# Kernel tuning notes

Measured on AMD Instinct MI355X. Metric: run time of the kernel, lower is better.

The kernel has to match this reference:

```python
import jax, jax.numpy as jnp
import numpy as np

PASSES = 6
S = 2           # numEdgeSets
D = 256         # inputLayerSize
OUT = 10        # outputLayerSize
HID = 80
B, N, E = 4, 10000, 160000


def _leaky(x):
    return jax.nn.leaky_relu(x, negative_slope=0.01)


def setup_inputs() -> dict:
    key = jax.random.key(0)
    ks = jax.random.split(key, 18)
    sc = 0.05
    return {
        "nodes": jax.random.normal(ks[0], (B, N, D), jnp.float32),
        "edges": jax.random.randint(ks[1], (B, S, E, 2), 0, N, jnp.int32),
        "problem_type": jax.random.uniform(ks[2], (B, 1), jnp.float32),
        # GRUCell params (torch layout: [3D, D] for ih and hh)
        "gru_w_ih": jax.random.normal(ks[3], (3 * D, D), jnp.float32) * sc,
        "gru_w_hh": jax.random.normal(ks[4], (3 * D, D), jnp.float32) * sc,
        "gru_b_ih": jax.random.normal(ks[5], (3 * D,), jnp.float32) * sc,
        "gru_b_hh": jax.random.normal(ks[6], (3 * D,), jnp.float32) * sc,
        # per-edge-set 2-layer MLP, stacked over edge sets
        "edge_w1": jax.random.normal(ks[7], (S, D, D), jnp.float32) * sc,
        "edge_b1": jax.random.normal(ks[8], (S, D), jnp.float32) * sc,
        "edge_w2": jax.random.normal(ks[9], (S, D, D), jnp.float32) * sc,
        "edge_b2": jax.random.normal(ks[10], (S, D), jnp.float32) * sc,
        # readout head
        "fc1_w": jax.random.normal(ks[11], (HID, D + 1), jnp.float32) * sc,
        "fc1_b": jax.random.normal(ks[12], (HID,), jnp.float32) * sc,
        "fc2_w": jax.random.normal(ks[13], (HID, HID), jnp.float32) * sc,
        "fc2_b": jax.random.normal(ks[14], (HID,), jnp.float32) * sc,
        "fc3_w": jax.random.normal(ks[15], (OUT, HID), jnp.float32) * sc,
        "fc3_b": jax.random.normal(ks[16], (OUT,), jnp.float32) * sc,
    }


def _gru_cell(x, h, w_ih, w_hh, b_ih, b_hh):
    # torch.nn.GRUCell semantics; x,h: [B,N,D]
    gi = jnp.einsum("bnd,ed->bne", x, w_ih) + b_ih   # [B,N,3D]
    gh = jnp.einsum("bnd,ed->bne", h, w_hh) + b_hh
    i_r, i_z, i_n = jnp.split(gi, 3, axis=-1)
    h_r, h_z, h_n = jnp.split(gh, 3, axis=-1)
    r = jax.nn.sigmoid(i_r + h_r)
    z = jax.nn.sigmoid(i_z + h_z)
    n = jnp.tanh(i_n + r * h_n)
    return (1.0 - z) * n + z * h


def reference(nodes, edges, problem_type, gru_w_ih, gru_w_hh, gru_b_ih, gru_b_hh,
              edge_w1, edge_b1, edge_w2, edge_b2,
              fc1_w, fc1_b, fc2_w, fc2_b, fc3_w, fc3_b):
    bidx = jnp.arange(B)[:, None]  # [B,1] for batched scatter
    h = nodes
    for j in range(PASSES):
        incoming = jnp.zeros_like(h)
        for si in range(S):
            dst = edges[:, si, :, 0]  # [B,E]
            src = edges[:, si, :, 1]  # [B,E]
            gathered = jnp.take_along_axis(h, src[:, :, None], axis=1)  # [B,E,D]
            y = _leaky(jnp.einsum("bed,fd->bef", gathered, edge_w1[si]) + edge_b1[si])
            y = jnp.einsum("bed,fd->bef", y, edge_w2[si]) + edge_b2[si]
            incoming = incoming.at[bidx, dst].add(y)
        h = _gru_cell(incoming, h, gru_w_ih, gru_w_hh, gru_b_ih, gru_b_hh)
        if j < PASSES - 2:
            h = jax.lax.stop_gradient(h)  # mirrors .detach()
    # graph readout: sum over nodes, log, nan->0, relu, +inf->finite max
    s = jnp.sum(h, axis=1)               # [B,D]
    l = jnp.log(s)
    l = jnp.where(jnp.isnan(l), 0.0, l)
    l = jax.nn.relu(l)
    finite_max = jnp.max(jnp.where(jnp.isinf(l), -jnp.inf, l), axis=1, keepdims=True)
    l = jnp.where(jnp.isinf(l), finite_max, l)
    x = jnp.concatenate([l, problem_type], axis=1)  # [B,D+1]
    x = _leaky(x @ fc1_w.T + fc1_b)
    x = _leaky(x @ fc2_w.T + fc2_b)
    return x @ fc3_w.T + fc3_b  # [B,OUT]
```

## Files before the change

kernel.cpp:

```cpp
#include <hip/hip_runtime.h>
#include <math.h>

#define NNODES 10000
#define NEDGES 160000
#define DIM    256
#define BATCH  4
#define NG     8
#define MROWS  40064
#define RBLK   625
#define RGRP   79
#define RBLK128 313
#define RGRP128 40

typedef __attribute__((ext_vector_type(8))) __bf16 bf16x8;
typedef __attribute__((ext_vector_type(4))) float  floatx4;
typedef __attribute__((ext_vector_type(8))) unsigned short ushort8v;

__device__ __forceinline__ float leakyf(float x){ return x > 0.f ? x : 0.01f*x; }
__device__ __forceinline__ float fsig(float x){ return 1.f/(1.f + __expf(-x)); }
__device__ __forceinline__ float ftanh(float x){ return 1.f - 2.f/(1.f + __expf(2.f*x)); }
__device__ __forceinline__ unsigned short f2bf_u(float x){
  unsigned int u = __float_as_uint(x);
  u += 0x7fffu + ((u >> 16) & 1u);
  return (unsigned short)(u >> 16);
}
__device__ __forceinline__ float bfdec(unsigned short u){
  return __uint_as_float(((unsigned int)u) << 16);
}
#define GATE_SCL 65535.f
#define GATE_INV 1.5259021896696422e-5f

#define VMCNT4 asm volatile("s_waitcnt vmcnt(4)" ::: "memory")
#define VMCNT3 asm volatile("s_waitcnt vmcnt(3)" ::: "memory")
#define VMCNT0 asm volatile("s_waitcnt vmcnt(0)" ::: "memory")
#define LGKM0  asm volatile("s_waitcnt lgkmcnt(0)" ::: "memory")
#define SBAR   __builtin_amdgcn_s_barrier()
#define SCHEDB __builtin_amdgcn_sched_barrier(0)

__device__ __forceinline__ void glds16(unsigned short* lds, const unsigned short* g){
  __builtin_amdgcn_global_load_lds(
      (const __attribute__((address_space(1))) void*)g,
      (__attribute__((address_space(3))) void*)lds, 16, 0, 0);
}

__global__ void ihinit_kernel(const float* __restrict__ nodes,
                              unsigned short* __restrict__ ihcat,
                              unsigned short* __restrict__ h_lo){
  int idx = blockIdx.x*256 + threadIdx.x;
  int row = idx >> 8, d = idx & 255;
  float v = nodes[idx];
  unsigned short h = f2bf_u(v);
  ihcat[(size_t)row*512 + 256 + d] = h;
  h_lo[idx] = f2bf_u(v - bfdec(h));
}

__global__ void w1cat_kernel(const float* __restrict__ ew1, unsigned short* __restrict__ o){
  int idx = blockIdx.x*256 + threadIdx.x;
  int n = idx >> 8, k = idx & 255;
  o[idx] = f2bf_u(ew1[(n>>8)*65536 + (n&255)*256 + k]);
}
__global__ void w2k_kernel(const float* __restrict__ ew2, unsigned short* __restrict__ o){
  int idx = blockIdx.x*256 + threadIdx.x;
  int n = idx >> 10, kp = idx & 1023;
  int j = kp & 511, term = kp >> 9;
  int si = j >> 8, k = j & 255;
  float v = ew2[si*65536 + n*256 + k];
  unsigned short h = f2bf_u(v);
  o[idx] = term ? f2bf_u(v - bfdec(h)) : h;
}
__global__ void wk2_kernel(const float* __restrict__ w, unsigned short* __restrict__ o){
  int idx = blockIdx.x*256 + threadIdx.x;
  int c = idx >> 9, kp = idx & 511;
  int k = kp & 255, term = kp >> 8;
  float v = w[c*256 + k];
  unsigned short h = f2bf_u(v);
  o[idx] = term ? f2bf_u(v - bfdec(h)) : h;
}
__global__ void wcomb_kernel(const float* __restrict__ wih, const float* __restrict__ whh,
                             unsigned short* __restrict__ o){
  int idx = blockIdx.x*256 + threadIdx.x;
  int c = idx >> 10, kp = idx & 1023;
  int seg = kp >> 8, k = kp & 255;
  const float* w = (seg & 1) ? whh : wih;
  float v = w[c*256 + k];
  unsigned short h = f2bf_u(v);
  o[idx] = (seg >> 1) ? f2bf_u(v - bfdec(h)) : h;
}

__global__ void hist_kernel(const int* __restrict__ edges, int* __restrict__ cnt){
  int idx = blockIdx.x*256 + threadIdx.x;
  if (idx < NG*NEDGES){
    int g = idx / NEDGES, e = idx - g*NEDGES;
    int d = edges[((size_t)g*NEDGES + e)*2];
    atomicAdd(&cnt[g*NNODES + d], 1);
  }
}

__global__ __launch_bounds__(256) void scan_kernel(const int* __restrict__ cnt, int* __restrict__ off){
  __shared__ int sc[256];
  int g = blockIdx.x, t = threadIdx.x;
  int base = 0;
  for (int c=0;c<40;c++){
    int i = c*256 + t;
    int v = (i < NNODES) ? cnt[g*NNODES + i] : 0;
    __syncthreads();
    sc[t] = v;
    __syncthreads();
    for (int o=1;o<256;o<<=1){
      int u = (t>=o) ? sc[t-o] : 0;
      __syncthreads();
      sc[t] += u;
      __syncthreads();
    }
    if (i < NNODES) off[g*(NNODES+1) + i] = base + sc[t] - v;
    base += sc[255];
  }
  if (t == 0) off[g*(NNODES+1) + NNODES] = base;
}

__global__ void scatter_kernel(const int* __restrict__ edges, const int* __restrict__ off,
                               int* __restrict__ cur, int* __restrict__ ssrc){
  int idx = blockIdx.x*256 + threadIdx.x;
  if (idx < NG*NEDGES){
    int g = idx / NEDGES, e = idx - g*NEDGES;
    const int* ep = &edges[((size_t)g*NEDGES + e)*2];
    int d = ep[0], s = ep[1];
    int pos = off[g*(NNODES+1) + d] + atomicAdd(&cur[g*NNODES + d], 1);
    ssrc[g*NEDGES + pos] = s;
  }
}

template<int KP, int RS, int KM>
__device__ __forceinline__ void mm128_core(
    const unsigned short* __restrict__ Ab, const unsigned short* __restrict__ Wb,
    unsigned short* lds, floatx4 (&acc)[4][2])
{
  const int t = threadIdx.x;
  const int w = t >> 6, lane = t & 63;
  const int q = lane >> 4, col = lane & 15;
  const int wr = (w >> 2) * 64;
  const int wc = (w & 3) * 32;
  const int sr = t >> 3;
  const int sk = ((t & 7) ^ (sr & 7)) * 8;

  auto STAGE = [&](int kb, int buf){
    unsigned short* Al = lds + buf*16384;
    unsigned short* Bl = Al + 8192;
    #pragma unroll
    for (int i=0;i<2;i++){
      int r = i*64 + sr;
      glds16(&Al[i*4096 + w*512], &Ab[(size_t)r*RS + ((kb + sk) & KM)]);
      glds16(&Bl[i*4096 + w*512], &Wb[(size_t)r*KP + kb + sk]);
    }
  };

  STAGE(0, 0);
  int cur = 0;
  #pragma unroll
  for (int kb = 0; kb < KP; kb += 64){
    if (kb + 64 < KP){
      STAGE(kb + 64, cur^1);
      VMCNT4;
    } else {
      VMCNT0;
    }
    SBAR; SCHEDB;
    const unsigned short* Al = lds + cur*16384;
    const unsigned short* Bl = Al + 8192;
    #pragma unroll
    for (int ks2=0; ks2<2; ks2++){
      bf16x8 a[4], bf[2];
      #pragma unroll
      for (int mi=0;mi<4;mi++){
        int r = wr + mi*16 + col;
        int j = (ks2*4 + q) ^ (r & 7);
        a[mi] = *(const bf16x8*)&Al[r*64 + j*8];
      }
      #pragma unroll
      for (int ni=0;ni<2;ni++){
        int r = wc + ni*16 + col;
        int j = (ks2*4 + q) ^ (r & 7);
        bf[ni] = *(const bf16x8*)&Bl[r*64 + j*8];
      }
      #pragma unroll
      for (int mi=0;mi<4;mi++)
        #pragma unroll
        for (int ni=0;ni<2;ni++)
          acc[mi][ni] = __builtin_amdgcn_mfma_f32_16x16x32_bf16(a[mi], bf[ni], acc[mi][ni], 0,0,0);
    }
    SCHEDB; LGKM0; SBAR;
    cur ^= 1;
  }
}

__device__ __forceinline__ void mm64x2_core(
    const unsigned short* __restrict__ A1, const unsigned short* __restrict__ W1,
    const unsigned short* __restrict__ A2, const unsigned short* __restrict__ W2,
    unsigned short* lds, floatx4 (&ai)[4], floatx4 (&ah)[4])
{
  const int t = threadIdx.x;
  const int w = t >> 6, lane = t & 63;
  const int q = lane >> 4, col = lane & 15;
  const int wc = w*16;
  const int sr = t >> 3;
  const int sk = ((t & 7) ^ (sr & 7)) * 8;

  auto STAGE = [&](int s, int buf){
    const unsigned short* A = (s < 8) ? A1 : A2;
    const unsigned short* W = (s < 8) ? W1 : W2;
    int kb = (s & 7) * 64;
    unsigned short* Al = lds + buf*12288;
    unsigned short* Bl = Al + 4096;
    glds16(&Al[w*512], &A[(size_t)sr*512 + ((kb + sk) & 255)]);
    #pragma unroll
    for (int i=0;i<2;i++){
      int r = i*64 + sr;
      glds16(&Bl[i*4096 + w*512], &W[(size_t)r*512 + kb + sk]);
    }
  };

  STAGE(0, 0);
  int cur = 0;
  #pragma unroll
  for (int s = 0; s < 16; s++){
    if (s < 15){
      STAGE(s + 1, cur^1);
      VMCNT3;
    } else {
      VMCNT0;
    }
    SBAR; SCHEDB;
    const unsigned short* Al = lds + cur*12288;
    const unsigned short* Bl = Al + 4096;
    #pragma unroll
    for (int ks2=0; ks2<2; ks2++){
      bf16x8 a[4], bf;
      #pragma unroll
      for (int mi=0;mi<4;mi++){
        int r = mi*16 + col;
        int j = (ks2*4 + q) ^ (r & 7);
        a[mi] = *(const bf16x8*)&Al[r*64 + j*8];
      }
      {
        int r = wc + col;
        int j = (ks2*4 + q) ^ (r & 7);
        bf = *(const bf16x8*)&Bl[r*64 + j*8];
      }
      if (s < 8){
        #pragma unroll
        for (int mi=0;mi<4;mi++)
          ai[mi] = __builtin_amdgcn_mfma_f32_16x16x32_bf16(a[mi], bf, ai[mi], 0,0,0);
      } else {
        #pragma unroll
        for (int mi=0;mi<4;mi++)
          ah[mi] = __builtin_amdgcn_mfma_f32_16x16x32_bf16(a[mi], bf, ah[mi], 0,0,0);
      }
    }
    SCHEDB; LGKM0; SBAR;
    cur ^= 1;
  }
}

#define XDECODE(NCOL) \
  const int bid_ = blockIdx.x; \
  const int rb_ = ((bid_ >> 3) / NCOL) * 8 + (bid_ & 7); \
  const int colb_ = (bid_ >> 3) % NCOL; \
  if (rb_ >= RBLK) return;

#define XDECODE128(NCOL) \
  const int bid_ = blockIdx.x; \
  const int rb_ = ((bid_ >> 3) / NCOL) * 8 + (bid_ & 7); \
  const int colb_ = (bid_ >> 3) % NCOL; \
  if (rb_ >= RBLK128) return;

#define MMPRO128 \
  const int t = threadIdx.x, w = t >> 6, lane = t & 63; \
  const int q = lane >> 4, col = lane & 15; \
  const int wrq = (w >> 2) * 64, wcq = (w & 3) * 32; \
  floatx4 acc[4][2]; \
  _Pragma("unroll") for (int mi=0;mi<4;mi++) _Pragma("unroll") for (int ni=0;ni<2;ni++) \
    acc[mi][ni] = (floatx4){0.f,0.f,0.f,0.f};

__global__ __launch_bounds__(512,4) void z64_kernel(
    const unsigned short* __restrict__ ihcat, const unsigned short* __restrict__ w1cat,
    const float* __restrict__ eb1, unsigned short* __restrict__ Z)
{
  __shared__ unsigned short lds[32768];
  XDECODE128(4)
  const int row0 = rb_*128, col0 = colb_*128;
  MMPRO128
  mm128_core<256,512,255>(ihcat + (size_t)row0*512 + 256, w1cat + (size_t)col0*256, lds, acc);

  #pragma unroll
  for (int ni=0;ni<2;ni++){
    int n = col0 + wcq + ni*16 + col;
    int si = n >> 8, cz = n & 255;
    float bb = eb1[si*256 + cz];
    unsigned short* zp = Z + (size_t)si*MROWS*256 + cz;
    #pragma unroll
    for (int mi=0;mi<4;mi++)
      #pragma unroll
      for (int rr=0;rr<4;rr++){
        int row = row0 + wrq + mi*16 + q*4 + rr;
        zp[(size_t)row*256] = f2bf_u(leakyf(acc[mi][ni][rr] + bb));
      }
  }
}

__global__ __launch_bounds__(256) void aggregate_kernel(
    const unsigned short* __restrict__ Z, const int* __restrict__ ssrc,
    const int* __restrict__ off, unsigned short* __restrict__ Sb)
{
  const int bid = blockIdx.x;
  const int g = bid & 7;
  const int dgrp = bid >> 3;
  const int b = g >> 1, si = g & 1;
  const int w = threadIdx.x >> 6, lane = threadIdx.x & 63;
  const int half = lane >> 5, c = lane & 31;
  const unsigned short* zb = Z + ((size_t)si*MROWS + b*10000)*256 + c*8;
  const int* sp = ssrc + (size_t)g*NEDGES;
  const int* offg = off + g*(NNODES+1);

  #pragma unroll
  for (int p=0;p<2;p++){
    const int d = dgrp*16 + w*4 + p*2 + half;
    int j = offg[d];
    const int j1 = offg[d+1];
    float a0=0.f,a1=0.f,a2=0.f,a3=0.f,a4=0.f,a5=0.f,a6=0.f,a7=0.f;
    for (; j+8 <= j1; j+=8){
      int s[8];
      #pragma unroll
      for (int e=0;e<8;e++) s[e] = sp[j+e];
      ushort8v u[8];
      #pragma unroll
      for (int e=0;e<8;e++) u[e] = *(const ushort8v*)&zb[(size_t)s[e]*256];
      a0 += bfdec(u[0][0])+bfdec(u[1][0])+bfdec(u[2][0])+bfdec(u[3][0]);
      a1 += bfdec(u[0][1])+bfdec(u[1][1])+bfdec(u[2][1])+bfdec(u[3][1]);
      a2 += bfdec(u[0][2])+bfdec(u[1][2])+bfdec(u[2][2])+bfdec(u[3][2]);
      a3 += bfdec(u[0][3])+bfdec(u[1][3])+bfdec(u[2][3])+bfdec(u[3][3]);
      a4 += bfdec(u[0][4])+bfdec(u[1][4])+bfdec(u[2][4])+bfdec(u[3][4]);
      a5 += bfdec(u[0][5])+bfdec(u[1][5])+bfdec(u[2][5])+bfdec(u[3][5]);
      a6 += bfdec(u[0][6])+bfdec(u[1][6])+bfdec(u[2][6])+bfdec(u[3][6]);
      a7 += bfdec(u[0][7])+bfdec(u[1][7])+bfdec(u[2][7])+bfdec(u[3][7]);
      a0 += bfdec(u[4][0])+bfdec(u[5][0])+bfdec(u[6][0])+bfdec(u[7][0]);
      a1 += bfdec(u[4][1])+bfdec(u[5][1])+bfdec(u[6][1])+bfdec(u[7][1]);
      a2 += bfdec(u[4][2])+bfdec(u[5][2])+bfdec(u[6][2])+bfdec(u[7][2]);
      a3 += bfdec(u[4][3])+bfdec(u[5][3])+bfdec(u[6][3])+bfdec(u[7][3]);
      a4 += bfdec(u[4][4])+bfdec(u[5][4])+bfdec(u[6][4])+bfdec(u[7][4]);
      a5 += bfdec(u[4][5])+bfdec(u[5][5])+bfdec(u[6][5])+bfdec(u[7][5]);
      a6 += bfdec(u[4][6])+bfdec(u[5][6])+bfdec(u[6][6])+bfdec(u[7][6]);
      a7 += bfdec(u[4][7])+bfdec(u[5][7])+bfdec(u[6][7])+bfdec(u[7][7]);
    }
    for (; j+4 <= j1; j+=4){
      int s0=sp[j], s1=sp[j+1], s2=sp[j+2], s3=sp[j+3];
      ushort8v u0 = *(const ushort8v*)&zb[(size_t)s0*256];
      ushort8v u1 = *(const ushort8v*)&zb[(size_t)s1*256];
      ushort8v u2 = *(const ushort8v*)&zb[(size_t)s2*256];
      ushort8v u3 = *(const ushort8v*)&zb[(size_t)s3*256];
      a0 += bfdec(u0[0])+bfdec(u1[0])+bfdec(u2[0])+bfdec(u3[0]);
      a1 += bfdec(u0[1])+bfdec(u1[1])+bfdec(u2[1])+bfdec(u3[1]);
      a2 += bfdec(u0[2])+bfdec(u1[2])+bfdec(u2[2])+bfdec(u3[2]);
      a3 += bfdec(u0[3])+bfdec(u1[3])+bfdec(u2[3])+bfdec(u3[3]);
      a4 += bfdec(u0[4])+bfdec(u1[4])+bfdec(u2[4])+bfdec(u3[4]);
      a5 += bfdec(u0[5])+bfdec(u1[5])+bfdec(u2[5])+bfdec(u3[5]);
      a6 += bfdec(u0[6])+bfdec(u1[6])+bfdec(u2[6])+bfdec(u3[6]);
      a7 += bfdec(u0[7])+bfdec(u1[7])+bfdec(u2[7])+bfdec(u3[7]);
    }
    for (; j < j1; j++){
      ushort8v u = *(const ushort8v*)&zb[(size_t)sp[j]*256];
      a0+=bfdec(u[0]); a1+=bfdec(u[1]); a2+=bfdec(u[2]); a3+=bfdec(u[3]);
      a4+=bfdec(u[4]); a5+=bfdec(u[5]); a6+=bfdec(u[6]); a7+=bfdec(u[7]);
    }
    size_t so = (size_t)(b*10000 + d)*512 + si*256 + c*8;
    ushort8v hv;
    hv[0]=f2bf_u(a0); hv[1]=f2bf_u(a1); hv[2]=f2bf_u(a2); hv[3]=f2bf_u(a3);
    hv[4]=f2bf_u(a4); hv[5]=f2bf_u(a5); hv[6]=f2bf_u(a6); hv[7]=f2bf_u(a7);
    *(ushort8v*)&Sb[so] = hv;
  }
}

__global__ __launch_bounds__(512,4) void w264_kernel(
    const unsigned short* __restrict__ Sb, const unsigned short* __restrict__ w2k,
    const float* __restrict__ eb2, const int* __restrict__ off,
    unsigned short* __restrict__ ihcat)
{
  __shared__ unsigned short lds[32768];
  XDECODE128(2)
  const int row0 = rb_*128, col0 = colb_*128;
  MMPRO128
  mm128_core<1024,512,511>(Sb + (size_t)row0*512, w2k + (size_t)col0*1024, lds, acc);

  float b20[2], b21[2];
  #pragma unroll
  for (int ni=0;ni<2;ni++){
    int n = col0 + wcq + ni*16 + col;
    b20[ni] = eb2[n];
    b21[ni] = eb2[256 + n];
  }
  #pragma unroll
  for (int mi=0;mi<4;mi++)
    #pragma unroll
    for (int rr=0;rr<4;rr++){
      int row = row0 + wrq + mi*16 + q*4 + rr;
      int rw = (row < 40000) ? row : 39999;
      int b = rw / 10000, d = rw - b*10000;
      int o0 = (b*2)*(NNODES+1) + d;
      int o1 = (b*2+1)*(NNODES+1) + d;
      float dg0 = (float)(off[o0+1] - off[o0]);
      float dg1 = (float)(off[o1+1] - off[o1]);
      #pragma unroll
      for (int ni=0;ni<2;ni++){
        int n = col0 + wcq + ni*16 + col;
        ihcat[(size_t)row*512 + n] = f2bf_u(acc[mi][ni][rr] + dg0*b20[ni] + dg1*b21[ni]);
      }
    }
}

__global__ __launch_bounds__(512,4) void gruA_kernel(
    const unsigned short* __restrict__ ihcat, const unsigned short* __restrict__ wcomb,
    const float* __restrict__ b_ih, const float* __restrict__ b_hh,
    unsigned short* __restrict__ rz_r, unsigned short* __restrict__ rz_z)
{
  __shared__ unsigned short lds[32768];
  XDECODE128(4)
  const int row0 = rb_*128, col0 = colb_*128;
  MMPRO128
  mm128_core<1024,512,511>(ihcat + (size_t)row0*512, wcomb + (size_t)col0*1024, lds, acc);

  float bb[2];
  #pragma unroll
  for (int ni=0;ni<2;ni++){
    int n = col0 + wcq + ni*16 + col;
    bb[ni] = b_ih[n] + b_hh[n];
  }
  unsigned short* dst = (col0 < 256) ? rz_r : rz_z;
  const int cbase = (col0 & 255) + wcq;
  #pragma unroll
  for (int mi=0;mi<4;mi++)
    #pragma unroll
    for (int rr=0;rr<4;rr++){
      size_t row = (size_t)(row0 + wrq + mi*16 + q*4 + rr);
      #pragma unroll
      for (int ni=0;ni<2;ni++){
        float v = fsig(acc[mi][ni][rr] + bb[ni]);
        dst[row*256 + cbase + ni*16 + col] = (unsigned short)(v*GATE_SCL + 0.5f);
      }
    }
}

__global__ __launch_bounds__(512,4) void gruB_kernel(
    const unsigned short* __restrict__ ihcat, unsigned short* __restrict__ h_lo,
    const unsigned short* __restrict__ wihk, const unsigned short* __restrict__ whhk,
    const float* __restrict__ b_ih, const float* __restrict__ b_hh,
    const unsigned short* __restrict__ rz_r, const unsigned short* __restrict__ rz_z,
    unsigned short* __restrict__ ihcat_nxt)
{
  __shared__ unsigned short lds[24576];
  XDECODE(2)
  const int row0 = rb_*64, dcol0 = colb_*128;
  const int t = threadIdx.x, w = t >> 6, lane = t & 63;
  const int q = lane >> 4, col = lane & 15;

  floatx4 ai[4], ah[4];
  #pragma unroll
  for (int mi=0;mi<4;mi++){ ai[mi] = (floatx4){0.f,0.f,0.f,0.f}; ah[mi] = (floatx4){0.f,0.f,0.f,0.f}; }

  mm64x2_core(ihcat + (size_t)row0*512,       wihk + (size_t)(512 + dcol0)*512,
              ihcat + (size_t)row0*512 + 256, whhk + (size_t)(512 + dcol0)*512,
              lds, ai, ah);

  const int dn = dcol0 + w*16 + col;
  const float bi = b_ih[512 + dn];
  const float bh = b_hh[512 + dn];
  #pragma unroll
  for (int mi=0;mi<4;mi++)
    #pragma unroll
    for (int rr=0;rr<4;rr++){
      size_t row = (size_t)(row0 + mi*16 + q*4 + rr);
      float rg = (float)rz_r[row*256 + dn] * GATE_INV;
      float zg = (float)rz_z[row*256 + dn] * GATE_INV;
      float ng = ftanh(ai[mi][rr] + bi + rg*(ah[mi][rr] + bh));
      float hv = bfdec(ihcat[row*512 + 256 + dn]) + bfdec(h_lo[row*256 + dn]);
      float hnew = (1.f - zg)*ng + zg*hv;
      unsigned short hh = f2bf_u(hnew);
      ihcat_nxt[row*512 + 256 + dn] = hh;
      h_lo[row*256 + dn] = f2bf_u(hnew - bfdec(hh));
    }
}

__global__ void reduce_kernel(const unsigned short* __restrict__ ihcat,
                              const unsigned short* __restrict__ h_lo,
                              float* __restrict__ sbuf){
  int b  = blockIdx.x / 50;
  int s0 = (blockIdx.x % 50) * 200;
  int d  = threadIdx.x;
  size_t row = (size_t)b*NNODES + s0;
  float acc = 0.f;
  for (int i=0;i<200;i++){
    acc += bfdec(ihcat[(row+i)*512 + 256 + d]) + bfdec(h_lo[(row+i)*256 + d]);
  }
  atomicAdd(&sbuf[b*DIM + d], acc);
}

__global__ __launch_bounds__(320) void head_kernel(
    const float* __restrict__ sbuf, const float* __restrict__ pt,
    const float* __restrict__ fc1w, const float* __restrict__ fc1b,
    const float* __restrict__ fc2w, const float* __restrict__ fc2b,
    const float* __restrict__ fc3w, const float* __restrict__ fc3b,
    float* __restrict__ out)
{
  __shared__ float L[4][257];
  __shared__ float T1[4][80];
  __shared__ float T2[4][80];
  __shared__ float fmx[4];
  int t = threadIdx.x;
  if (t < 256){
    for (int b=0;b<4;b++){
      float v = sbuf[b*DIM + t];
      float ll = logf(v);
      if (ll != ll) ll = 0.f;
      ll = fmaxf(ll, 0.f);
      L[b][t] = ll;
    }
  }
  __syncthreads();
  int w = t >> 6, lane = t & 63;
  if (w < 4){
    float m = -INFINITY;
    for (int i=lane;i<256;i+=64){ float v = L[w][i]; if (v != INFINITY) m = fmaxf(m, v); }
    #pragma unroll
    for (int o=32;o>=1;o>>=1) m = fmaxf(m, __shfl_xor(m, o, 64));
    if (lane==0) fmx[w] = m;
  }
  __syncthreads();
  if (t < 256){
    for (int b=0;b<4;b++) if (L[b][t] == INFINITY) L[b][t] = fmx[b];
  }
  if (t < 4) L[t][256] = pt[t];
  __syncthreads();
  if (t < 320){
    int b = t/80, i = t%80;
    float a = fc1b[i];
    for (int k=0;k<257;k++) a += L[b][k]*fc1w[i*257+k];
    T1[b][i] = leakyf(a);
  }
  __syncthreads();
  if (t < 320){
    int b = t/80, i = t%80;
    float a = fc2b[i];
    for (int k=0;k<80;k++) a += T1[b][k]*fc2w[i*80+k];
    T2[b][i] = leakyf(a);
  }
  __syncthreads();
  if (t < 40){
    int b = t/10, i = t%10;
    float a = fc3b[i];
    for (int k=0;k<80;k++) a += T2[b][k]*fc3w[i*80+k];
    out[b*10+i] = a;
  }
}

extern "C" void kernel_launch(void* const* d_in, const int* in_sizes, int n_in,
                              void* d_out, int out_size, void* d_ws, size_t ws_size,
                              hipStream_t stream) {
  const float* nodes = (const float*)d_in[0];
  const int*   edges = (const int*)d_in[1];
  const float* pt    = (const float*)d_in[2];
  const float* w_ih  = (const float*)d_in[3];
  const float* w_hh  = (const float*)d_in[4];
  const float* b_ih  = (const float*)d_in[5];
  const float* b_hh  = (const float*)d_in[6];
  const float* ew1   = (const float*)d_in[7];
  const float* eb1   = (const float*)d_in[8];
  const float* ew2   = (const float*)d_in[9];
  const float* eb2   = (const float*)d_in[10];
  const float* fc1w  = (const float*)d_in[11];
  const float* fc1b  = (const float*)d_in[12];
  const float* fc2w  = (const float*)d_in[13];
  const float* fc2b  = (const float*)d_in[14];
  const float* fc3w  = (const float*)d_in[15];
  const float* fc3b  = (const float*)d_in[16];

  const size_t HN  = (size_t)BATCH*NNODES*DIM;
  const size_t HNP = (size_t)MROWS*DIM;
  char* p = (char*)d_ws;
  float* sbuf = (float*)p;                        p += BATCH*DIM*4;
  unsigned short* ihcat0 = (unsigned short*)p;    p += (size_t)MROWS*512*2;
  unsigned short* ihcat1 = (unsigned short*)p;    p += (size_t)MROWS*512*2;
  unsigned short* h_lo   = (unsigned short*)p;    p += HNP*2;
  unsigned short* Zb   = (unsigned short*)p;      p += 2*HNP*2;
  unsigned short* Sb   = (unsigned short*)p;      p += (size_t)MROWS*512*2;
  unsigned short* w1cat= (unsigned short*)p;      p += 512*256*2;
  unsigned short* w2k  = (unsigned short*)p;      p += 256*1024*2;
  unsigned short* wihk = (unsigned short*)p;      p += 768*512*2;
  unsigned short* whhk = (unsigned short*)p;      p += 768*512*2;
  unsigned short* wcomb= (unsigned short*)p;      p += 512*1024*2;
  int* off  = (int*)p;                            p += NG*(NNODES+1)*4;
  int* cur  = (int*)p;                            p += NG*NNODES*4;
  int* ssrc = (int*)p;                            p += (size_t)NG*NEDGES*4;

  unsigned short* rz_r = (unsigned short*)Sb;
  unsigned short* rz_z = rz_r + (size_t)MROWS*256;

  w1cat_kernel<<<512,256,0,stream>>>(ew1, w1cat);
  w2k_kernel<<<1024,256,0,stream>>>(ew2, w2k);
  wk2_kernel<<<1536,256,0,stream>>>(w_ih, wihk);
  wk2_kernel<<<1536,256,0,stream>>>(w_hh, whhk);
  wcomb_kernel<<<2048,256,0,stream>>>(w_ih, w_hh, wcomb);

  ihinit_kernel<<<(int)(HN/256),256,0,stream>>>(nodes, ihcat0, h_lo);

  hipMemsetAsync(cur, 0, NG*NNODES*sizeof(int), stream);
  hist_kernel<<<(NG*NEDGES)/256,256,0,stream>>>(edges, cur);
  scan_kernel<<<NG,256,0,stream>>>(cur, off);
  hipMemsetAsync(cur, 0, NG*NNODES*sizeof(int), stream);
  scatter_kernel<<<(NG*NEDGES)/256,256,0,stream>>>(edges, off, cur, ssrc);

  hipMemsetAsync(sbuf, 0, BATCH*DIM*sizeof(float), stream);

  unsigned short* ih[2] = {ihcat0, ihcat1};

  for (int pass=0; pass<6; pass++){
    unsigned short* curb = ih[pass & 1];
    unsigned short* nxtb = ih[(pass+1) & 1];
    z64_kernel<<<RGRP128*8*4,512,0,stream>>>(curb, w1cat, eb1, Zb);
    aggregate_kernel<<<5000,256,0,stream>>>(Zb, ssrc, off, Sb);
    w264_kernel<<<RGRP128*8*2,512,0,stream>>>(Sb, w2k, eb2, off, curb);
    gruA_kernel<<<RGRP128*8*4,512,0,stream>>>(curb, wcomb, b_ih, b_hh, rz_r, rz_z);
    gruB_kernel<<<RGRP*8*2,512,0,stream>>>(curb, h_lo, wihk, whhk, b_ih, b_hh,
                                           rz_r, rz_z, nxtb);
  }
  reduce_kernel<<<200,256,0,stream>>>(ih[0], h_lo, sbuf);
  head_kernel<<<1,320,0,stream>>>(sbuf, pt, fc1w,fc1b,fc2w,fc2b,fc3w,fc3b,(float*)d_out);
}
```

Before: 1.567 ms.

## Parallelize CSR prefix scan, vectorize ihinit, deepen aggregate unroll to 16

The single-block-per-graph serial scan becomes a two-phase multi-block scan: per-chunk block scans, then a pass that adds chunk offsets. ihinit now processes four elements per thread with float4 loads and ushort4 stores. hist and scatter interleave graphs across blocks and drop the bounds check. The aggregate gather loop now issues 16 row loads per iteration instead of 8, raising memory-level parallelism at the cost of more registers. The tsum scratch reuses sbuf, which is zeroed afterwards.

```diff
diff --git a/kernel.cpp b/kernel.cpp
--- a/kernel.cpp
+++ b/kernel.cpp
@@ -47,11 +47,18 @@
                               unsigned short* __restrict__ ihcat,
                               unsigned short* __restrict__ h_lo){
   int idx = blockIdx.x*256 + threadIdx.x;
-  int row = idx >> 8, d = idx & 255;
-  float v = nodes[idx];
-  unsigned short h = f2bf_u(v);
-  ihcat[(size_t)row*512 + 256 + d] = h;
-  h_lo[idx] = f2bf_u(v - bfdec(h));
+  int base = idx*4;
+  int row = base >> 8, d = base & 255;
+  float4 v = *(const float4*)&nodes[base];
+  unsigned short h0=f2bf_u(v.x), h1=f2bf_u(v.y), h2=f2bf_u(v.z), h3=f2bf_u(v.w);
+  ushort4 hi; hi.x=h0; hi.y=h1; hi.z=h2; hi.w=h3;
+  *(ushort4*)&ihcat[(size_t)row*512 + 256 + d] = hi;
+  ushort4 lo;
+  lo.x = f2bf_u(v.x - bfdec(h0));
+  lo.y = f2bf_u(v.y - bfdec(h1));
+  lo.z = f2bf_u(v.z - bfdec(h2));
+  lo.w = f2bf_u(v.w - bfdec(h3));
+  *(ushort4*)&h_lo[base] = lo;
 }
 
 __global__ void w1cat_kernel(const float* __restrict__ ew1, unsigned short* __restrict__ o){
@@ -88,46 +95,61 @@
 }
 
 __global__ void hist_kernel(const int* __restrict__ edges, int* __restrict__ cnt){
-  int idx = blockIdx.x*256 + threadIdx.x;
-  if (idx < NG*NEDGES){
-    int g = idx / NEDGES, e = idx - g*NEDGES;
-    int d = edges[((size_t)g*NEDGES + e)*2];
-    atomicAdd(&cnt[g*NNODES + d], 1);
-  }
-}
-
-__global__ __launch_bounds__(256) void scan_kernel(const int* __restrict__ cnt, int* __restrict__ off){
+  int bid = blockIdx.x;
+  int g = bid & 7, chunk = bid >> 3;
+  int e = chunk*256 + threadIdx.x;
+  int d = edges[((size_t)g*NEDGES + e)*2];
+  atomicAdd(&cnt[g*NNODES + d], 1);
+}
+
+__global__ __launch_bounds__(256) void scanA_kernel(const int* __restrict__ cnt,
+                                                    int* __restrict__ off,
+                                                    int* __restrict__ tsum){
   __shared__ int sc[256];
-  int g = blockIdx.x, t = threadIdx.x;
+  int bid = blockIdx.x;
+  int g = bid & 7, c = bid >> 3;
+  int t = threadIdx.x;
+  int i = c*256 + t;
+  int v = (i < NNODES) ? cnt[g*NNODES + i] : 0;
+  sc[t] = v;
+  __syncthreads();
+  for (int o=1;o<256;o<<=1){
+    int u = (t>=o) ? sc[t-o] : 0;
+    __syncthreads();
+    sc[t] += u;
+    __syncthreads();
+  }
+  if (i < NNODES) off[g*(NNODES+1) + i] = sc[t] - v;
+  if (t == 255) tsum[g*40 + c] = sc[255];
+}
+__global__ __launch_bounds__(256) void scanC_kernel(const int* __restrict__ tsum,
+                                                    int* __restrict__ off){
+  __shared__ int ts[40];
+  int bid = blockIdx.x;
+  int g = bid & 7, c = bid >> 3;
+  int t = threadIdx.x;
+  if (t < 40) ts[t] = tsum[g*40 + t];
+  __syncthreads();
   int base = 0;
-  for (int c=0;c<40;c++){
-    int i = c*256 + t;
-    int v = (i < NNODES) ? cnt[g*NNODES + i] : 0;
-    __syncthreads();
-    sc[t] = v;
-    __syncthreads();
-    for (int o=1;o<256;o<<=1){
-      int u = (t>=o) ? sc[t-o] : 0;
-      __syncthreads();
-      sc[t] += u;
-      __syncthreads();
-    }
-    if (i < NNODES) off[g*(NNODES+1) + i] = base + sc[t] - v;
-    base += sc[255];
-  }
-  if (t == 0) off[g*(NNODES+1) + NNODES] = base;
+  for (int k=0;k<40;k++) base += (k < c) ? ts[k] : 0;
+  int i = c*256 + t;
+  if (i < NNODES) off[g*(NNODES+1) + i] += base;
+  if (c == 39 && t == 0){
+    int tot = 0;
+    for (int k=0;k<40;k++) tot += ts[k];
+    off[g*(NNODES+1) + NNODES] = tot;
+  }
 }
 
 __global__ void scatter_kernel(const int* __restrict__ edges, const int* __restrict__ off,
                                int* __restrict__ cur, int* __restrict__ ssrc){
-  int idx = blockIdx.x*256 + threadIdx.x;
-  if (idx < NG*NEDGES){
-    int g = idx / NEDGES, e = idx - g*NEDGES;
-    const int* ep = &edges[((size_t)g*NEDGES + e)*2];
-    int d = ep[0], s = ep[1];
-    int pos = off[g*(NNODES+1) + d] + atomicAdd(&cur[g*NNODES + d], 1);
-    ssrc[g*NEDGES + pos] = s;
-  }
+  int bid = blockIdx.x;
+  int g = bid & 7, chunk = bid >> 3;
+  int e = chunk*256 + threadIdx.x;
+  const int* ep = &edges[((size_t)g*NEDGES + e)*2];
+  int d = ep[0], s = ep[1];
+  int pos = off[g*(NNODES+1) + d] + atomicAdd(&cur[g*NNODES + d], 1);
+  ssrc[g*NEDGES + pos] = s;
 }
 
 template<int KP, int RS, int KM>
@@ -306,6 +328,17 @@
       }
   }
 }
+
+#define ACC4(B) do { \
+  a0 += bfdec(u[B][0])+bfdec(u[B+1][0])+bfdec(u[B+2][0])+bfdec(u[B+3][0]); \
+  a1 += bfdec(u[B][1])+bfdec(u[B+1][1])+bfdec(u[B+2][1])+bfdec(u[B+3][1]); \
+  a2 += bfdec(u[B][2])+bfdec(u[B+1][2])+bfdec(u[B+2][2])+bfdec(u[B+3][2]); \
+  a3 += bfdec(u[B][3])+bfdec(u[B+1][3])+bfdec(u[B+2][3])+bfdec(u[B+3][3]); \
+  a4 += bfdec(u[B][4])+bfdec(u[B+1][4])+bfdec(u[B+2][4])+bfdec(u[B+3][4]); \
+  a5 += bfdec(u[B][5])+bfdec(u[B+1][5])+bfdec(u[B+2][5])+bfdec(u[B+3][5]); \
+  a6 += bfdec(u[B][6])+bfdec(u[B+1][6])+bfdec(u[B+2][6])+bfdec(u[B+3][6]); \
+  a7 += bfdec(u[B][7])+bfdec(u[B+1][7])+bfdec(u[B+2][7])+bfdec(u[B+3][7]); \
+} while(0)
 
 __global__ __launch_bounds__(256) void aggregate_kernel(
     const unsigned short* __restrict__ Z, const int* __restrict__ ssrc,
@@ -327,49 +360,28 @@
     int j = offg[d];
     const int j1 = offg[d+1];
     float a0=0.f,a1=0.f,a2=0.f,a3=0.f,a4=0.f,a5=0.f,a6=0.f,a7=0.f;
-    for (; j+8 <= j1; j+=8){
-      int s[8];
-      #pragma unroll
-      for (int e=0;e<8;e++) s[e] = sp[j+e];
-      ushort8v u[8];
-      #pragma unroll
-      for (int e=0;e<8;e++) u[e] = *(const ushort8v*)&zb[(size_t)s[e]*256];
-      a0 += bfdec(u[0][0])+bfdec(u[1][0])+bfdec(u[2][0])+bfdec(u[3][0]);
-      a1 += bfdec(u[0][1])+bfdec(u[1][1])+bfdec(u[2][1])+bfdec(u[3][1]);
-      a2 += bfdec(u[0][2])+bfdec(u[1][2])+bfdec(u[2][2])+bfdec(u[3][2]);
-      a3 += bfdec(u[0][3])+bfdec(u[1][3])+bfdec(u[2][3])+bfdec(u[3][3]);
-      a4 += bfdec(u[0][4])+bfdec(u[1][4])+bfdec(u[2][4])+bfdec(u[3][4]);
-      a5 += bfdec(u[0][5])+bfdec(u[1][5])+bfdec(u[2][5])+bfdec(u[3][5]);
-      a6 += bfdec(u[0][6])+bfdec(u[1][6])+bfdec(u[2][6])+bfdec(u[3][6]);
-      a7 += bfdec(u[0][7])+bfdec(u[1][7])+bfdec(u[2][7])+bfdec(u[3][7]);
-      a0 += bfdec(u[4][0])+bfdec(u[5][0])+bfdec(u[6][0])+bfdec(u[7][0]);
-      a1 += bfdec(u[4][1])+bfdec(u[5][1])+bfdec(u[6][1])+bfdec(u[7][1]);
-      a2 += bfdec(u[4][2])+bfdec(u[5][2])+bfdec(u[6][2])+bfdec(u[7][2]);
-      a3 += bfdec(u[4][3])+bfdec(u[5][3])+bfdec(u[6][3])+bfdec(u[7][3]);
-      a4 += bfdec(u[4][4])+bfdec(u[5][4])+bfdec(u[6][4])+bfdec(u[7][4]);
-      a5 += bfdec(u[4][5])+bfdec(u[5][5])+bfdec(u[6][5])+bfdec(u[7][5]);
-      a6 += bfdec(u[4][6])+bfdec(u[5][6])+bfdec(u[6][6])+bfdec(u[7][6]);
-      a7 += bfdec(u[4][7])+bfdec(u[5][7])+bfdec(u[6][7])+bfdec(u[7][7]);
+    for (; j+16 <= j1; j+=16){
+      int s[16];
+      #pragma unroll
+      for (int e=0;e<16;e++) s[e] = sp[j+e];
+      ushort8v u[16];
+      #pragma unroll
+      for (int e=0;e<16;e++) u[e] = *(const ushort8v*)&zb[(size_t)s[e]*256];
+      ACC4(0); ACC4(4); ACC4(8); ACC4(12);
     }
     for (; j+4 <= j1; j+=4){
-      int s0=sp[j], s1=sp[j+1], s2=sp[j+2], s3=sp[j+3];
-      ushort8v u0 = *(const ushort8v*)&zb[(size_t)s0*256];
-      ushort8v u1 = *(const ushort8v*)&zb[(size_t)s1*256];
-      ushort8v u2 = *(const ushort8v*)&zb[(size_t)s2*256];
-      ushort8v u3 = *(const ushort8v*)&zb[(size_t)s3*256];
-      a0 += bfdec(u0[0])+bfdec(u1[0])+bfdec(u2[0])+bfdec(u3[0]);
-      a1 += bfdec(u0[1])+bfdec(u1[1])+bfdec(u2[1])+bfdec(u3[1]);
-      a2 += bfdec(u0[2])+bfdec(u1[2])+bfdec(u2[2])+bfdec(u3[2]);
-      a3 += bfdec(u0[3])+bfdec(u1[3])+bfdec(u2[3])+bfdec(u3[3]);
-      a4 += bfdec(u0[4])+bfdec(u1[4])+bfdec(u2[4])+bfdec(u3[4]);
-      a5 += bfdec(u0[5])+bfdec(u1[5])+bfdec(u2[5])+bfdec(u3[5]);
-      a6 += bfdec(u0[6])+bfdec(u1[6])+bfdec(u2[6])+bfdec(u3[6]);
-      a7 += bfdec(u0[7])+bfdec(u1[7])+bfdec(u2[7])+bfdec(u3[7]);
+      int s[4];
+      #pragma unroll
+      for (int e=0;e<4;e++) s[e] = sp[j+e];
+      ushort8v u[4];
+      #pragma unroll
+      for (int e=0;e<4;e++) u[e] = *(const ushort8v*)&zb[(size_t)s[e]*256];
+      ACC4(0);
     }
     for (; j < j1; j++){
-      ushort8v u = *(const ushort8v*)&zb[(size_t)sp[j]*256];
-      a0+=bfdec(u[0]); a1+=bfdec(u[1]); a2+=bfdec(u[2]); a3+=bfdec(u[3]);
-      a4+=bfdec(u[4]); a5+=bfdec(u[5]); a6+=bfdec(u[6]); a7+=bfdec(u[7]);
+      ushort8v uu = *(const ushort8v*)&zb[(size_t)sp[j]*256];
+      a0+=bfdec(uu[0]); a1+=bfdec(uu[1]); a2+=bfdec(uu[2]); a3+=bfdec(uu[3]);
+      a4+=bfdec(uu[4]); a5+=bfdec(uu[5]); a6+=bfdec(uu[6]); a7+=bfdec(uu[7]);
     }
     size_t so = (size_t)(b*10000 + d)*512 + si*256 + c*8;
     ushort8v hv;
@@ -601,6 +613,7 @@
 
   unsigned short* rz_r = (unsigned short*)Sb;
   unsigned short* rz_z = rz_r + (size_t)MROWS*256;
+  int* tsum = (int*)sbuf;
 
   w1cat_kernel<<<512,256,0,stream>>>(ew1, w1cat);
   w2k_kernel<<<1024,256,0,stream>>>(ew2, w2k);
@@ -608,11 +621,12 @@
   wk2_kernel<<<1536,256,0,stream>>>(w_hh, whhk);
   wcomb_kernel<<<2048,256,0,stream>>>(w_ih, w_hh, wcomb);
 
-  ihinit_kernel<<<(int)(HN/256),256,0,stream>>>(nodes, ihcat0, h_lo);
+  ihinit_kernel<<<(int)(HN/1024),256,0,stream>>>(nodes, ihcat0, h_lo);
 
   hipMemsetAsync(cur, 0, NG*NNODES*sizeof(int), stream);
   hist_kernel<<<(NG*NEDGES)/256,256,0,stream>>>(edges, cur);
-  scan_kernel<<<NG,256,0,stream>>>(cur, off);
+  scanA_kernel<<<NG*40,256,0,stream>>>(cur, off, tsum);
+  scanC_kernel<<<NG*40,256,0,stream>>>(tsum, off);
   hipMemsetAsync(cur, 0, NG*NNODES*sizeof(int), stream);
   scatter_kernel<<<(NG*NEDGES)/256,256,0,stream>>>(edges, off, cur, ssrc);
 
```

Measured after the change: 1.510 ms. 1.04x faster.
